# Kernel tuning notes

Measured on AMD Instinct MI355X. Metric: run time of the kernel, lower is better.

The kernel has to match this reference:

```python
import jax, jax.numpy as jnp
import numpy as np

N_NODES = 50000
N_EDGES = 800000
N_RELS = 16
D = 128


def _rgcn_layer(h, W, b, loop_w, gate_w, src, dst, rel, norm, apply_relu, n_nodes):
    # Transform all node features by every relation weight once: [R, N, D_out].
    # Equivalent to DGL bmm_maybe_select's per-edge W[rel] bmm, but avoids an
    # [E, D, D] gather of weights.
    h_all = jnp.einsum('nd,rde->rne', h, W)
    msg = h_all[rel, src]                                    # [E, D_out]
    msg = msg * norm                                         # edge norm scaling
    gate_logit = jnp.einsum('nd,rd->rn', h, gate_w[..., 0])  # [R, N]
    gate = jax.nn.sigmoid(gate_logit[rel, src])[:, None]     # [E, 1]
    msg = msg * gate
    agg = jax.ops.segment_sum(msg, dst, num_segments=n_nodes)  # fn.sum -> dst
    out = agg + b + h @ loop_w                               # bias + self loop
    if apply_relu:
        out = jax.nn.relu(out)
    return out  # dropout is identity in eval mode


def setup_inputs() -> dict:
    key = jax.random.key(0)
    ks = jax.random.split(key, 12)
    gain = float(np.sqrt(2.0))  # relu gain (xavier-ish scale; values arbitrary)
    def xav(k, shape):
        fan = shape[-2] + shape[-1]
        s = gain * np.sqrt(6.0 / fan)
        return jax.random.uniform(k, shape, jnp.float32, -s, s)
    return {
        'h': jax.random.normal(ks[0], (N_NODES, D), jnp.float32),
        'norm': jax.random.uniform(ks[1], (N_EDGES, 1), jnp.float32),
        'weight0': xav(ks[2], (N_RELS, D, D)),
        'bias0': jnp.zeros((D,), jnp.float32),
        'loop_w0': xav(ks[3], (D, D)),
        'gate_w0': xav(ks[4], (N_RELS, D, 1)),
        'weight1': xav(ks[5], (N_RELS, D, D)),
        'bias1': jnp.zeros((D,), jnp.float32),
        'loop_w1': xav(ks[6], (D, D)),
        'gate_w1': xav(ks[7], (N_RELS, D, 1)),
        'src': jax.random.randint(ks[8], (N_EDGES,), 0, N_NODES, jnp.int32),
        'dst': jax.random.randint(ks[9], (N_EDGES,), 0, N_NODES, jnp.int32),
        'rel_type': jax.random.randint(ks[10], (N_EDGES,), 0, N_RELS, jnp.int32),
    }


def reference(h, norm, weight0, bias0, loop_w0, gate_w0,
              weight1, bias1, loop_w1, gate_w1, src, dst, rel_type):
    n_nodes = h.shape[0]
    # Layer 0: activation=relu (idx < num_hidden_layers - 1)
    h = _rgcn_layer(h, weight0, bias0, loop_w0, gate_w0, src, dst, rel_type,
                    norm, True, n_nodes)
    # Layer 1: no activation
    h = _rgcn_layer(h, weight1, bias1, loop_w1, gate_w1, src, dst, rel_type,
                    norm, False, n_nodes)
    return h
```

## Files before the change

### kernel.cpp

```cpp
#include <hip/hip_runtime.h>
#include <hip/hip_bf16.h>
#include <stdint.h>

#define NN 50000
#define NE 800000
#define NR 16
#define SCAN_NB ((NN + 255) / 256)
#define NTILES ((NN + 127) / 128)

typedef unsigned short u16;
typedef unsigned int u32;

typedef __bf16 bf16x8 __attribute__((ext_vector_type(8)));
typedef float f32x4 __attribute__((ext_vector_type(4)));

__device__ __forceinline__ u16 f2bf(float f) {
  u32 u = __float_as_uint(f);
  u = u + 0x7FFFu + ((u >> 16) & 1u);
  return (u16)(u >> 16);
}

__global__ void hist_kernel(const int* __restrict__ dst, int* __restrict__ counts) {
  int e = blockIdx.x * 256 + threadIdx.x;
  if (e < NE) atomicAdd(&counts[dst[e]], 1);
}

__global__ void scan_partial(const int* __restrict__ counts, int* __restrict__ bsum) {
  __shared__ int buf[256];
  int t = threadIdx.x;
  int i = blockIdx.x * 256 + t;
  int v = (i < NN) ? counts[i] : 0;
  buf[t] = v;
  __syncthreads();
  for (int off = 1; off < 256; off <<= 1) {
    int x = buf[t];
    int y = (t >= off) ? buf[t - off] : 0;
    __syncthreads();
    buf[t] = x + y;
    __syncthreads();
  }
  if (t == 255) bsum[blockIdx.x] = buf[255];
}

__global__ void scan_blocksums(const int* __restrict__ bsum, int* __restrict__ boff,
                               int* __restrict__ starts) {
  __shared__ int buf[256];
  int t = threadIdx.x;
  buf[t] = (t < SCAN_NB) ? bsum[t] : 0;
  __syncthreads();
  for (int off = 1; off < 256; off <<= 1) {
    int x = buf[t];
    int y = (t >= off) ? buf[t - off] : 0;
    __syncthreads();
    buf[t] = x + y;
    __syncthreads();
  }
  if (t < SCAN_NB) boff[t] = buf[t] - bsum[t];
  if (t == 255) starts[NN] = buf[255];
}

__global__ void scan_final(const int* __restrict__ counts, const int* __restrict__ boff,
                           int* __restrict__ starts, int* __restrict__ cursor) {
  __shared__ int buf[256];
  int t = threadIdx.x;
  int i = blockIdx.x * 256 + t;
  int v = (i < NN) ? counts[i] : 0;
  buf[t] = v;
  __syncthreads();
  for (int off = 1; off < 256; off <<= 1) {
    int x = buf[t];
    int y = (t >= off) ? buf[t - off] : 0;
    __syncthreads();
    buf[t] = x + y;
    __syncthreads();
  }
  int s = boff[blockIdx.x] + buf[t] - v;
  if (i < NN) {
    starts[i] = s;
    cursor[i] = s;
  }
}

__global__ void scatter_kernel(const int* __restrict__ src, const int* __restrict__ dst,
                               const int* __restrict__ rel, const float* __restrict__ norm,
                               int* __restrict__ cursor, uint2* __restrict__ esd) {
  int e = blockIdx.x * 256 + threadIdx.x;
  if (e < NE) {
    int d = dst[e];
    int pos = atomicAdd(&cursor[d], 1);
    esd[pos] = make_uint2(((u32)rel[e] << 16) | (u32)src[e], __float_as_uint(norm[e]));
  }
}

__global__ void convert_wt(const float* __restrict__ w0, const float* __restrict__ lw0,
                           const float* __restrict__ w1, const float* __restrict__ lw1,
                           u16* __restrict__ Wt) {
  int m = blockIdx.y;
  int idx = blockIdx.x * 256 + threadIdx.x;
  int d = idx >> 7, k = idx & 127;
  const float* s;
  if (m < 16) s = w0 + (size_t)m * 16384;
  else if (m == 16) s = lw0;
  else if (m < 33) s = w1 + (size_t)(m - 17) * 16384;
  else s = lw1;
  Wt[(size_t)m * 16384 + idx] = f2bf(s[k * 128 + d]);
}

__global__ void hconv_kernel(const float* __restrict__ h, u16* __restrict__ hbf) {
  int i = blockIdx.x * 256 + threadIdx.x;
  float4 v = ((const float4*)h)[i];
  ushort4 u;
  u.x = f2bf(v.x); u.y = f2bf(v.y); u.z = f2bf(v.z); u.w = f2bf(v.w);
  ((ushort4*)hbf)[i] = u;
}

__global__ void gates_kernel(const float* __restrict__ h, const float* __restrict__ gw,
                             float* __restrict__ gates) {
  __shared__ float hs[16 * 132];
  __shared__ float gws[16 * 132];
  int t = threadIdx.x;
  int n0 = blockIdx.x * 16;
#pragma unroll
  for (int i = 0; i < 2; ++i) {
    int f = t + 256 * i;
    int row = f >> 5, c4 = (f & 31) * 4;
    *(float4*)&hs[row * 132 + c4] = *(const float4*)&h[(size_t)(n0 + row) * 128 + c4];
    *(float4*)&gws[row * 132 + c4] = *(const float4*)&gw[row * 128 + c4];
  }
  __syncthreads();
  int nl = t >> 4, r = t & 15;
  float s = 0.f;
#pragma unroll 8
  for (int k = 0; k < 128; ++k) s += hs[nl * 132 + k] * gws[r * 132 + k];
  gates[r * NN + n0 + nl] = 1.f / (1.f + __expf(-s));
}

template <bool WF32>
__global__ __launch_bounds__(256, 2)
void transform_kernel(const u16* __restrict__ hbf, const u16* __restrict__ Wt,
                      int cnt, int CM, const float* __restrict__ gate_base,
                      u16* __restrict__ tmp, float* __restrict__ fout,
                      const float* __restrict__ bias) {
  __shared__ u16 As[128 * 136];
  __shared__ u16 Bs[128 * 136];
  __shared__ float gs[128];
  int t = threadIdx.x;
  int n0 = blockIdx.x * 128;
#pragma unroll
  for (int i = 0; i < 8; ++i) {
    int u8 = t + 256 * i;
    int row = u8 >> 4, c8 = (u8 & 15) * 8;
    int n = n0 + row;
    uint4 v = make_uint4(0, 0, 0, 0);
    if (n < NN) v = *(const uint4*)&hbf[(size_t)n * 128 + c8];
    *(uint4*)&As[row * 136 + c8] = v;
  }
  int wave = t >> 6, lane = t & 63;
  int wr = (wave >> 1) * 64, wc = (wave & 1) * 64;
  int mrow = lane & 15, quad = lane >> 4;
  int m0 = blockIdx.y * CM;
  int m1 = m0 + CM < cnt ? m0 + CM : cnt;
  for (int m = m0; m < m1; ++m) {
    __syncthreads();
#pragma unroll
    for (int i = 0; i < 8; ++i) {
      int u8 = t + 256 * i;
      int row = u8 >> 4, c8 = (u8 & 15) * 8;
      *(uint4*)&Bs[row * 136 + c8] = *(const uint4*)&Wt[(size_t)m * 16384 + row * 128 + c8];
    }
    if (!WF32 && t < 128) {
      int n = n0 + t;
      gs[t] = (n < NN) ? gate_base[(size_t)m * NN + n] : 0.f;
    }
    __syncthreads();
    f32x4 acc[4][4];
#pragma unroll
    for (int i = 0; i < 4; ++i)
#pragma unroll
      for (int j = 0; j < 4; ++j) acc[i][j] = (f32x4){0.f, 0.f, 0.f, 0.f};
#pragma unroll
    for (int kk = 0; kk < 4; ++kk) {
      int k0 = kk * 32 + quad * 8;
      bf16x8 a[4], b[4];
#pragma unroll
      for (int i = 0; i < 4; ++i) a[i] = *(const bf16x8*)&As[(wr + i * 16 + mrow) * 136 + k0];
#pragma unroll
      for (int j = 0; j < 4; ++j) b[j] = *(const bf16x8*)&Bs[(wc + j * 16 + mrow) * 136 + k0];
#pragma unroll
      for (int i = 0; i < 4; ++i)
#pragma unroll
        for (int j = 0; j < 4; ++j)
          acc[i][j] = __builtin_amdgcn_mfma_f32_16x16x32_bf16(a[i], b[j], acc[i][j], 0, 0, 0);
    }
#pragma unroll
    for (int i = 0; i < 4; ++i) {
#pragma unroll
      for (int r = 0; r < 4; ++r) {
        int row = wr + i * 16 + quad * 4 + r;
        int n = n0 + row;
        if (n < NN) {
          float g = WF32 ? 0.f : gs[row];
#pragma unroll
          for (int j = 0; j < 4; ++j) {
            int col = wc + j * 16 + mrow;
            float v = acc[i][j][r];
            if (WF32) fout[(size_t)n * 128 + col] = v + bias[col];
            else tmp[((size_t)m * NN + n) * 128 + col] = f2bf(v * g);
          }
        }
      }
    }
  }
}

template <bool FULL>
__global__ __launch_bounds__(256)
void aggregate_kernel(const u32* __restrict__ tmp, const uint2* __restrict__ esd,
                      const int* __restrict__ starts, float* __restrict__ hout,
                      int mat_lo, int mat_cnt, int relu) {
  int wave = threadIdx.x >> 6, lane = threadIdx.x & 63;
  int v = blockIdx.x * 4 + wave;
  if (v >= NN) return;
  int s = starts[v], e = starts[v + 1];
  float a0 = 0.f, a1 = 0.f;
  int j = s;
  if (FULL) {
    for (; j + 8 <= e; j += 8) {
      uint2 p[8];
      u32 w[8];
      float sc[8];
#pragma unroll
      for (int i = 0; i < 8; ++i) p[i] = esd[j + i];
#pragma unroll
      for (int i = 0; i < 8; ++i) {
        u32 rs = p[i].x;
        u32 off = ((rs >> 16) * (u32)NN + (rs & 0xFFFFu)) * 64u + (u32)lane;
        w[i] = tmp[off];
        sc[i] = __uint_as_float(p[i].y);
      }
#pragma unroll
      for (int i = 0; i < 8; ++i) {
        a0 = fmaf(sc[i], __uint_as_float(w[i] << 16), a0);
        a1 = fmaf(sc[i], __uint_as_float(w[i] & 0xFFFF0000u), a1);
      }
    }
  }
  for (; j < e; ++j) {
    uint2 p = esd[j];
    int rel = (int)(p.x >> 16);
    u32 rl = (u32)(rel - mat_lo);
    if (FULL || rl < (u32)mat_cnt) {
      u32 off = (rl * (u32)NN + (p.x & 0xFFFFu)) * 64u + (u32)lane;
      float sc = __uint_as_float(p.y);
      u32 w = tmp[off];
      a0 = fmaf(sc, __uint_as_float(w << 16), a0);
      a1 = fmaf(sc, __uint_as_float(w & 0xFFFF0000u), a1);
    }
  }
  float2* ho = (float2*)&hout[(size_t)v * 128 + lane * 2];
  float2 b = *ho;
  float o0 = b.x + a0, o1 = b.y + a1;
  if (relu) { o0 = fmaxf(o0, 0.f); o1 = fmaxf(o1, 0.f); }
  *ho = make_float2(o0, o1);
}

static void run_layer(const float* hin, u16* hbf, const u16* Wt, int wt_base,
                      const float* gw, const float* bias, float* hout,
                      u16* tmp, const uint2* esd, float* gates, const int* starts,
                      int mats_per_chunk, int relu, hipStream_t stream) {
  hconv_kernel<<<NN * 32 / 256, 256, 0, stream>>>(hin, hbf);
  gates_kernel<<<NN / 16, 256, 0, stream>>>(hin, gw, gates);
  transform_kernel<true><<<dim3(NTILES, 1), 256, 0, stream>>>(
      hbf, Wt + (size_t)(wt_base + 16) * 16384, 1, 1, nullptr, nullptr, hout, bias);
  for (int lo = 0; lo < NR; lo += mats_per_chunk) {
    int cnt = NR - lo < mats_per_chunk ? NR - lo : mats_per_chunk;
    const int CM = 2;
    int G = (cnt + CM - 1) / CM;
    transform_kernel<false><<<dim3(NTILES, G), 256, 0, stream>>>(
        hbf, Wt + (size_t)(wt_base + lo) * 16384, cnt, CM, gates + (size_t)lo * NN,
        tmp, nullptr, nullptr);
    int last = (lo + cnt >= NR);
    if (cnt == NR)
      aggregate_kernel<true><<<(NN + 3) / 4, 256, 0, stream>>>(
          (const u32*)tmp, esd, starts, hout, 0, NR, relu && last);
    else
      aggregate_kernel<false><<<(NN + 3) / 4, 256, 0, stream>>>(
          (const u32*)tmp, esd, starts, hout, lo, cnt, relu && last);
  }
}

extern "C" void kernel_launch(void* const* d_in, const int* in_sizes, int n_in,
                              void* d_out, int out_size, void* d_ws, size_t ws_size,
                              hipStream_t stream) {
  const float* h0   = (const float*)d_in[0];
  const float* norm = (const float*)d_in[1];
  const float* w0   = (const float*)d_in[2];
  const float* b0   = (const float*)d_in[3];
  const float* lw0  = (const float*)d_in[4];
  const float* gw0  = (const float*)d_in[5];
  const float* w1   = (const float*)d_in[6];
  const float* b1   = (const float*)d_in[7];
  const float* lw1  = (const float*)d_in[8];
  const float* gw1  = (const float*)d_in[9];
  const int*   src  = (const int*)d_in[10];
  const int*   dst  = (const int*)d_in[11];
  const int*   rel  = (const int*)d_in[12];
  float* out = (float*)d_out;

  char* p = (char*)d_ws;
  auto alloc = [&](size_t bytes) -> void* {
    void* q = (void*)p;
    p += (bytes + 255) & ~(size_t)255;
    return q;
  };
  u16*   Wt     = (u16*)alloc((size_t)34 * 16384 * 2);
  float* gates  = (float*)alloc((size_t)NR * NN * 4);
  float* h1     = (float*)alloc((size_t)NN * 128 * 4);
  u16*   hbf    = (u16*)alloc((size_t)NN * 128 * 2);
  int*   counts = (int*)alloc((size_t)NN * 4);
  int*   cursor = (int*)alloc((size_t)NN * 4);
  int*   starts = (int*)alloc((size_t)(NN + 1) * 4);
  int*   bsum   = (int*)alloc((size_t)256 * 4);
  int*   boff   = (int*)alloc((size_t)256 * 4);
  uint2* esd    = (uint2*)alloc((size_t)NE * 8);
  size_t used = (size_t)(p - (char*)d_ws);
  size_t per_mat = (size_t)NN * 128 * 2;
  int mats = (int)((ws_size > used ? ws_size - used : 0) / per_mat);
  if (mats > NR) mats = NR;
  if (mats < 1) mats = 1;
  u16* tmp = (u16*)alloc((size_t)mats * per_mat);

  hipMemsetAsync(counts, 0, (size_t)NN * 4, stream);
  hist_kernel<<<NE / 256, 256, 0, stream>>>(dst, counts);
  scan_partial<<<SCAN_NB, 256, 0, stream>>>(counts, bsum);
  scan_blocksums<<<1, 256, 0, stream>>>(bsum, boff, starts);
  scan_final<<<SCAN_NB, 256, 0, stream>>>(counts, boff, starts, cursor);
  scatter_kernel<<<NE / 256, 256, 0, stream>>>(src, dst, rel, norm, cursor, esd);
  convert_wt<<<dim3(64, 34), 256, 0, stream>>>(w0, lw0, w1, lw1, Wt);

  run_layer(h0, hbf, Wt, 0,  gw0, b0, h1,  tmp, esd, gates, starts, mats, 1, stream);
  run_layer(h1, hbf, Wt, 17, gw1, b1, out, tmp, esd, gates, starts, mats, 0, stream);
}
```

Baseline: 520.0 us.

## Swap GEMM operand roles to vectorize epilogue stores and read weights directly

```diff
diff --git a/kernel.cpp b/kernel.cpp
--- a/kernel.cpp
+++ b/kernel.cpp
@@ -12,12 +12,24 @@
 typedef unsigned int u32;
 
 typedef __bf16 bf16x8 __attribute__((ext_vector_type(8)));
+typedef __bf16 bf16x2 __attribute__((ext_vector_type(2)));
 typedef float f32x4 __attribute__((ext_vector_type(4)));
 
 __device__ __forceinline__ u16 f2bf(float f) {
   u32 u = __float_as_uint(f);
   u = u + 0x7FFFu + ((u >> 16) & 1u);
   return (u16)(u >> 16);
+}
+
+__device__ __forceinline__ u32 pk2bf(float x, float y) {
+#if __has_builtin(__builtin_amdgcn_cvt_pk_bf16_f32)
+  bf16x2 r = __builtin_amdgcn_cvt_pk_bf16_f32(x, y);
+  union { bf16x2 v; u32 u; } c;
+  c.v = r;
+  return c.u;
+#else
+  return (u32)f2bf(x) | ((u32)f2bf(y) << 16);
+#endif
 }
 
 __global__ void hist_kernel(const int* __restrict__ dst, int* __restrict__ counts) {
@@ -136,14 +148,12 @@
 }
 
 template <bool WF32>
-__global__ __launch_bounds__(256, 2)
+__global__ __launch_bounds__(256, 3)
 void transform_kernel(const u16* __restrict__ hbf, const u16* __restrict__ Wt,
                       int cnt, int CM, const float* __restrict__ gate_base,
                       u16* __restrict__ tmp, float* __restrict__ fout,
                       const float* __restrict__ bias) {
   __shared__ u16 As[128 * 136];
-  __shared__ u16 Bs[128 * 136];
-  __shared__ float gs[128];
   int t = threadIdx.x;
   int n0 = blockIdx.x * 128;
 #pragma unroll
@@ -155,24 +165,27 @@
     if (n < NN) v = *(const uint4*)&hbf[(size_t)n * 128 + c8];
     *(uint4*)&As[row * 136 + c8] = v;
   }
+  __syncthreads();
   int wave = t >> 6, lane = t & 63;
-  int wr = (wave >> 1) * 64, wc = (wave & 1) * 64;
+  int wd = (wave & 1) * 64, wn = (wave >> 1) * 64;
   int mrow = lane & 15, quad = lane >> 4;
+  float4 bv[4];
+  if (WF32) {
+#pragma unroll
+    for (int i = 0; i < 4; ++i) bv[i] = *(const float4*)&bias[wd + i * 16 + quad * 4];
+  }
   int m0 = blockIdx.y * CM;
   int m1 = m0 + CM < cnt ? m0 + CM : cnt;
   for (int m = m0; m < m1; ++m) {
-    __syncthreads();
-#pragma unroll
-    for (int i = 0; i < 8; ++i) {
-      int u8 = t + 256 * i;
-      int row = u8 >> 4, c8 = (u8 & 15) * 8;
-      *(uint4*)&Bs[row * 136 + c8] = *(const uint4*)&Wt[(size_t)m * 16384 + row * 128 + c8];
-    }
-    if (!WF32 && t < 128) {
-      int n = n0 + t;
-      gs[t] = (n < NN) ? gate_base[(size_t)m * NN + n] : 0.f;
-    }
-    __syncthreads();
+    const u16* wp = Wt + (size_t)m * 16384;
+    float g[4];
+    if (!WF32) {
+#pragma unroll
+      for (int j = 0; j < 4; ++j) {
+        int n = n0 + wn + j * 16 + mrow;
+        g[j] = (n < NN) ? gate_base[(size_t)m * NN + n] : 0.f;
+      }
+    }
     f32x4 acc[4][4];
 #pragma unroll
     for (int i = 0; i < 4; ++i)
@@ -183,9 +196,11 @@
       int k0 = kk * 32 + quad * 8;
       bf16x8 a[4], b[4];
 #pragma unroll
-      for (int i = 0; i < 4; ++i) a[i] = *(const bf16x8*)&As[(wr + i * 16 + mrow) * 136 + k0];
-#pragma unroll
-      for (int j = 0; j < 4; ++j) b[j] = *(const bf16x8*)&Bs[(wc + j * 16 + mrow) * 136 + k0];
+      for (int i = 0; i < 4; ++i)
+        a[i] = *(const bf16x8*)&wp[(wd + i * 16 + mrow) * 128 + k0];
+#pragma unroll
+      for (int j = 0; j < 4; ++j)
+        b[j] = *(const bf16x8*)&As[(wn + j * 16 + mrow) * 136 + k0];
 #pragma unroll
       for (int i = 0; i < 4; ++i)
 #pragma unroll
@@ -193,19 +208,24 @@
           acc[i][j] = __builtin_amdgcn_mfma_f32_16x16x32_bf16(a[i], b[j], acc[i][j], 0, 0, 0);
     }
 #pragma unroll
-    for (int i = 0; i < 4; ++i) {
-#pragma unroll
-      for (int r = 0; r < 4; ++r) {
-        int row = wr + i * 16 + quad * 4 + r;
-        int n = n0 + row;
-        if (n < NN) {
-          float g = WF32 ? 0.f : gs[row];
-#pragma unroll
-          for (int j = 0; j < 4; ++j) {
-            int col = wc + j * 16 + mrow;
-            float v = acc[i][j][r];
-            if (WF32) fout[(size_t)n * 128 + col] = v + bias[col];
-            else tmp[((size_t)m * NN + n) * 128 + col] = f2bf(v * g);
+    for (int j = 0; j < 4; ++j) {
+      int n = n0 + wn + j * 16 + mrow;
+      if (n < NN) {
+#pragma unroll
+        for (int i = 0; i < 4; ++i) {
+          int d0 = wd + i * 16 + quad * 4;
+          if (WF32) {
+            float4 v;
+            v.x = acc[i][j][0] + bv[i].x;
+            v.y = acc[i][j][1] + bv[i].y;
+            v.z = acc[i][j][2] + bv[i].z;
+            v.w = acc[i][j][3] + bv[i].w;
+            *(float4*)&fout[(size_t)n * 128 + d0] = v;
+          } else {
+            uint2 st;
+            st.x = pk2bf(acc[i][j][0] * g[j], acc[i][j][1] * g[j]);
+            st.y = pk2bf(acc[i][j][2] * g[j], acc[i][j][3] * g[j]);
+            *(uint2*)&tmp[((size_t)m * NN + n) * 128 + d0] = st;
           }
         }
       }
@@ -314,7 +334,7 @@
     return q;
   };
   u16*   Wt     = (u16*)alloc((size_t)34 * 16384 * 2);
-  float* gates  = (float*)alloc((size_t)NR * NN * 4);
+  float* gates  = (float*)alloc(((size_t)NR * NN + 256) * 4);
   float* h1     = (float*)alloc((size_t)NN * 128 * 4);
   u16*   hbf    = (u16*)alloc((size_t)NN * 128 * 2);
   int*   counts = (int*)alloc((size_t)NN * 4);
```

New measurement: 721.5 us. 1.39x slower.
